# Performance work log

Measured on AMD Instinct MI355X. Metric: run time of the kernel, lower is better.

Reference implementation:

```python
import jax, jax.numpy as jnp
from jax import lax
import numpy as np

DN = ('NCHW', 'OIHW', 'NCHW')


def _conv(x, w, b, stride, pad):
    y = lax.conv_general_dilated(x, w, (stride, stride), [(pad, pad), (pad, pad)],
                                 dimension_numbers=DN)
    return y + b[None, :, None, None]


def _conv_t(x, w, b):
    # torch ConvTranspose2d(k=4, stride=2, padding=1) equivalent:
    # lhs_dilation=2, effective padding k-1-p = 2 on each side -> output 2H x 2W
    y = lax.conv_general_dilated(x, w, (1, 1), [(2, 2), (2, 2)],
                                 lhs_dilation=(2, 2), dimension_numbers=DN)
    return y + b[None, :, None, None]


def setup_inputs() -> dict:
    key = jax.random.key(0)
    ks = jax.random.split(key, 16)
    D, K = 8, 512  # latent_dim, codebook_size

    def w(k, shape, fan_in):
        return jax.random.normal(k, shape, jnp.float32) * (1.0 / np.sqrt(fan_in))

    inp = {
        'x': jax.random.uniform(ks[0], (32, 3, 256, 256), jnp.float32),
        # encoder
        'enc_w1': w(ks[1], (32, 3, 4, 4), 3 * 16), 'enc_b1': jnp.zeros((32,), jnp.float32),
        'enc_w2': w(ks[2], (64, 32, 4, 4), 32 * 16), 'enc_b2': jnp.zeros((64,), jnp.float32),
        'enc_w3': w(ks[3], (D, 64, 1, 1), 64), 'enc_b3': jnp.zeros((D,), jnp.float32),
        # codebook, uniform(-1/K, 1/K) as in torch init
        'codebook': jax.random.uniform(ks[4], (K, D), jnp.float32, -1.0 / K, 1.0 / K),
        # decoder
        'dec_w1': w(ks[5], (64, D, 3, 3), D * 9), 'dec_b1': jnp.zeros((64,), jnp.float32),
        'dect_w1': w(ks[6], (64, 64, 4, 4), 64 * 16), 'dect_b1': jnp.zeros((64,), jnp.float32),
        'dect_w2': w(ks[7], (32, 64, 4, 4), 64 * 16), 'dect_b2': jnp.zeros((32,), jnp.float32),
        'dec_w2': w(ks[8], (3, 32, 3, 3), 32 * 9), 'dec_b2': jnp.zeros((3,), jnp.float32),
    }
    return inp


def reference(x, enc_w1, enc_b1, enc_w2, enc_b2, enc_w3, enc_b3, codebook,
              dec_w1, dec_b1, dect_w1, dect_b1, dect_w2, dect_b2, dec_w2, dec_b2):
    commitment_cost = 0.25
    B = x.shape[0]
    D = codebook.shape[1]

    # encoder
    h = jax.nn.relu(_conv(x, enc_w1, enc_b1, 2, 1))
    h = jax.nn.relu(_conv(h, enc_w2, enc_b2, 2, 1))
    z = _conv(h, enc_w3, enc_b3, 1, 0)                      # [B, D, H/4, W/4]

    # VQ: pairwise squared distances, argmin, gather
    z_flat = z.transpose(0, 2, 3, 1).reshape(-1, D)          # [N, D] in NHWC order
    distances = (jnp.sum(z_flat ** 2, axis=1, keepdims=True)
                 + jnp.sum(codebook ** 2, axis=1)
                 - 2.0 * z_flat @ codebook.T)                 # [N, K]
    encoding_indices = jnp.argmin(distances, axis=1)          # [N]
    # NOTE: faithful to original bug - reshaped directly into NCHW without permute
    z_q = codebook[encoding_indices].reshape(z.shape)

    commitment_loss = jnp.mean((z - lax.stop_gradient(z_q)) ** 2)
    codebook_loss = jnp.mean((z_q - lax.stop_gradient(z)) ** 2)
    vq_loss = codebook_loss + commitment_cost * commitment_loss

    # straight-through estimator
    z_q = z + lax.stop_gradient(z_q - z)

    # decoder
    h = jax.nn.relu(_conv(z_q, dec_w1, dec_b1, 1, 1))
    h = jax.nn.relu(_conv_t(h, dect_w1, dect_b1))
    h = jax.nn.relu(_conv_t(h, dect_w2, dect_b2))
    x_recon = jax.nn.sigmoid(_conv(h, dec_w2, dec_b2, 1, 1))

    return x_recon, vq_loss, encoding_indices.reshape(B, -1)
```

## Files before the change

kernel.cpp:

```cpp
#include <hip/hip_runtime.h>
#include <hip/hip_bf16.h>
#include <math.h>


__device__ __forceinline__ int rfl(int v) { return __builtin_amdgcn_readfirstlane(v); }

typedef __attribute__((ext_vector_type(8))) short s8v;
typedef __attribute__((ext_vector_type(4))) float f4v;

__device__ __forceinline__ ushort f2bf(float f) {
    __hip_bfloat16 h = __float2bfloat16(f);
    return *(ushort*)&h;
}

__global__ __launch_bounds__(256) void k_conv1(const float* __restrict__ x, const float* __restrict__ w,
                                               const float* __restrict__ bias, float* __restrict__ out) {
    int t = blockIdx.x * 256 + threadIdx.x;
    int ow  = t & 127;
    int oh0 = ((t >> 7) & 31) * 4;
    int co0 = rfl((t >> 12) & 15);
    int b   = rfl(t >> 16);
    float acc[4][2] = {};
    for (int ci = 0; ci < 3; ci++) {
        const float* xp  = x + (b * 3 + ci) * 65536;
        const float* wpA = w + (co0 * 3 + ci) * 16;
        const float* wpB = w + ((co0 + 16) * 3 + ci) * 16;
        #pragma unroll
        for (int r = 0; r < 10; r++) {
            int ih = oh0 * 2 - 1 + r;
            bool rok = (ih >= 0) && (ih < 256);
            int ihc = rok ? ih : 0;
            float v[4];
            #pragma unroll
            for (int c = 0; c < 4; c++) {
                int iw = ow * 2 - 1 + c;
                bool ok = rok && (iw >= 0) && (iw < 256);
                int iwc = iw < 0 ? 0 : (iw > 255 ? 255 : iw);
                float vv = xp[ihc * 256 + iwc];
                v[c] = ok ? vv : 0.f;
            }
            #pragma unroll
            for (int o = 0; o < 4; o++) {
                int kh = r - 2 * o;
                if (kh >= 0 && kh < 4) {
                    #pragma unroll
                    for (int kw = 0; kw < 4; kw++) {
                        acc[o][0] = __builtin_fmaf(v[kw], wpA[kh * 4 + kw], acc[o][0]);
                        acc[o][1] = __builtin_fmaf(v[kw], wpB[kh * 4 + kw], acc[o][1]);
                    }
                }
            }
        }
    }
    float bA = bias[co0], bB = bias[co0 + 16];
    #pragma unroll
    for (int o = 0; o < 4; o++) {
        float vA = acc[o][0] + bA, vB = acc[o][1] + bB;
        out[((b * 32 + co0) * 128 + oh0 + o) * 128 + ow]      = vA > 0.f ? vA : 0.f;
        out[((b * 32 + co0 + 16) * 128 + oh0 + o) * 128 + ow] = vB > 0.f ? vB : 0.f;
    }
}

__global__ __launch_bounds__(256) void k_conv2t(const float* __restrict__ h1, const float* __restrict__ w,
                                                const float* __restrict__ bias, float* __restrict__ out) {
    __shared__ float P[32][18][2][10];
    int bx = blockIdx.x;
    int b  = bx >> 6;
    int ty = (bx >> 3) & 7, tx = bx & 7;
    int oh0 = ty * 8, ow0 = tx * 8;
    int tid = threadIdx.x;
    for (int i = tid; i < 10368; i += 256) {
        int ci = i / 324, rem = i - ci * 324;
        int r = rem / 18, c = rem - r * 18;
        int ih = oh0 * 2 - 1 + r, iw = ow0 * 2 - 1 + c;
        float v = 0.f;
        if (ih >= 0 && ih < 128 && iw >= 0 && iw < 128)
            v = h1[(b * 32 + ci) * 16384 + ih * 128 + iw];
        P[ci][r][c & 1][c >> 1] = v;
    }
    __syncthreads();
    int lane = tid & 63;
    int dy = lane >> 3, dx = lane & 7;
    int co_base = rfl((tid >> 6) * 16);
    int oh = oh0 + dy, ow = ow0 + dx;
    for (int cc = 0; cc < 4; cc++) {
        int co0 = co_base + cc * 4;
        float a0 = 0.f, a1 = 0.f, a2 = 0.f, a3 = 0.f;
        for (int ci = 0; ci < 32; ci++) {
            const float* wp0 = w + ((co0 + 0) * 32 + ci) * 16;
            const float* wp1 = w + ((co0 + 1) * 32 + ci) * 16;
            const float* wp2 = w + ((co0 + 2) * 32 + ci) * 16;
            const float* wp3 = w + ((co0 + 3) * 32 + ci) * 16;
            #pragma unroll
            for (int kh = 0; kh < 4; kh++) {
                int r = 2 * dy + kh;
                float v0 = P[ci][r][0][dx];
                float v1 = P[ci][r][1][dx];
                float v2 = P[ci][r][0][dx + 1];
                float v3 = P[ci][r][1][dx + 1];
                a0 = __builtin_fmaf(v0, wp0[kh*4+0], a0); a0 = __builtin_fmaf(v1, wp0[kh*4+1], a0);
                a0 = __builtin_fmaf(v2, wp0[kh*4+2], a0); a0 = __builtin_fmaf(v3, wp0[kh*4+3], a0);
                a1 = __builtin_fmaf(v0, wp1[kh*4+0], a1); a1 = __builtin_fmaf(v1, wp1[kh*4+1], a1);
                a1 = __builtin_fmaf(v2, wp1[kh*4+2], a1); a1 = __builtin_fmaf(v3, wp1[kh*4+3], a1);
                a2 = __builtin_fmaf(v0, wp2[kh*4+0], a2); a2 = __builtin_fmaf(v1, wp2[kh*4+1], a2);
                a2 = __builtin_fmaf(v2, wp2[kh*4+2], a2); a2 = __builtin_fmaf(v3, wp2[kh*4+3], a2);
                a3 = __builtin_fmaf(v0, wp3[kh*4+0], a3); a3 = __builtin_fmaf(v1, wp3[kh*4+1], a3);
                a3 = __builtin_fmaf(v2, wp3[kh*4+2], a3); a3 = __builtin_fmaf(v3, wp3[kh*4+3], a3);
            }
        }
        float r0 = a0 + bias[co0 + 0], r1 = a1 + bias[co0 + 1];
        float r2 = a2 + bias[co0 + 2], r3 = a3 + bias[co0 + 3];
        out[((b * 64 + co0 + 0) * 64 + oh) * 64 + ow] = r0 > 0.f ? r0 : 0.f;
        out[((b * 64 + co0 + 1) * 64 + oh) * 64 + ow] = r1 > 0.f ? r1 : 0.f;
        out[((b * 64 + co0 + 2) * 64 + oh) * 64 + ow] = r2 > 0.f ? r2 : 0.f;
        out[((b * 64 + co0 + 3) * 64 + oh) * 64 + ow] = r3 > 0.f ? r3 : 0.f;
    }
}

__global__ __launch_bounds__(256) void k_conv3(const float* __restrict__ h2, const float* __restrict__ w,
                                               const float* __restrict__ bias, float* __restrict__ zf) {
    __shared__ float wl[8][64];
    __shared__ float bl[8];
    int tid = threadIdx.x;
    for (int i = tid; i < 512; i += 256) wl[i >> 6][i & 63] = w[i];
    if (tid < 8) bl[tid] = bias[tid];
    __syncthreads();
    int t = blockIdx.x * 256 + tid;
    int b = t >> 12, hw = t & 4095;
    float acc[8];
    for (int d = 0; d < 8; d++) acc[d] = 0.f;
    for (int ci = 0; ci < 64; ci++) {
        float v = h2[(b * 64 + ci) * 4096 + hw];
        for (int d = 0; d < 8; d++) acc[d] = __builtin_fmaf(v, wl[d][ci], acc[d]);
    }
    for (int d = 0; d < 8; d++)
        zf[(b * 8 + d) * 4096 + hw] = acc[d] + bl[d];
}

__global__ __launch_bounds__(256) void k_vq(const float* __restrict__ zf, const float* __restrict__ cb,
                                            int* __restrict__ idx, float* __restrict__ out_idx) {
    __shared__ float cbs[512][8];
    __shared__ float c2s[512];
    int tid = threadIdx.x;
    for (int i = tid; i < 4096; i += 256) cbs[i >> 3][i & 7] = cb[i];
    __syncthreads();
    for (int k = tid; k < 512; k += 256) {
        float s = 0.f;
        for (int d = 0; d < 8; d++) {
            float c = cbs[k][d];
            s = s + __fmul_rn(c, c);
        }
        c2s[k] = s;
    }
    __syncthreads();
    int n = blockIdx.x * 256 + tid;
    int b = n >> 12, hw = n & 4095;
    float zv[8], s1 = 0.f;
    for (int d = 0; d < 8; d++) {
        float z = zf[(b * 8 + d) * 4096 + hw];
        zv[d] = z;
        s1 = s1 + __fmul_rn(z, z);
    }
    float best = 3.4e38f; int bi = 0;
    for (int k = 0; k < 512; k++) {
        float dot = 0.f;
        for (int d = 0; d < 8; d++) dot = __builtin_fmaf(zv[d], cbs[k][d], dot);
        float a = s1 + c2s[k];
        float dist = a - __fmul_rn(2.0f, dot);
        if (dist < best) { best = dist; bi = k; }
    }
    idx[n] = bi;
    out_idx[n] = (float)bi;
}

__global__ __launch_bounds__(256) void k_zq(const int* __restrict__ idx, const float* __restrict__ cb,
                                            const float* __restrict__ zf, float* __restrict__ zq,
                                            double* __restrict__ partial) {
    __shared__ double red[256];
    int t = blockIdx.x * 256 + threadIdx.x;
    float q = cb[idx[t >> 3] * 8 + (t & 7)];
    zq[t] = q;
    double d = (double)zf[t] - (double)q;
    red[threadIdx.x] = d * d;
    __syncthreads();
    for (int s = 128; s > 0; s >>= 1) {
        if (threadIdx.x < s) red[threadIdx.x] += red[threadIdx.x + s];
        __syncthreads();
    }
    if (threadIdx.x == 0) partial[blockIdx.x] = red[0];
}

__global__ __launch_bounds__(256) void k_loss_fin(const double* __restrict__ partial, float* __restrict__ out_loss) {
    __shared__ double red[256];
    double s = 0.0;
    for (int i = threadIdx.x; i < 4096; i += 256) s += partial[i];
    red[threadIdx.x] = s;
    __syncthreads();
    for (int st = 128; st > 0; st >>= 1) {
        if (threadIdx.x < st) red[threadIdx.x] += red[threadIdx.x + st];
        __syncthreads();
    }
    if (threadIdx.x == 0)
        out_loss[0] = (float)(1.25 * red[0] / 1048576.0);
}

__global__ __launch_bounds__(256) void k_dec1(const float* __restrict__ zq, const float* __restrict__ w,
                                              const float* __restrict__ bias, float* __restrict__ out) {
    int t = blockIdx.x * 256 + threadIdx.x;
    int ow  = t & 63;
    int oh0 = ((t >> 6) & 15) * 4;
    int co0 = rfl((t >> 10) & 31);
    int b   = rfl(t >> 15);
    float acc[4][2] = {};
    for (int ci = 0; ci < 8; ci++) {
        const float* ip  = zq + (b * 8 + ci) * 4096;
        const float* wpA = w + (co0 * 8 + ci) * 9;
        const float* wpB = w + ((co0 + 32) * 8 + ci) * 9;
        #pragma unroll
        for (int r = 0; r < 6; r++) {
            int ih = oh0 - 1 + r;
            bool rok = (ih >= 0) && (ih < 64);
            int ihc = rok ? ih : 0;
            float v[3];
            #pragma unroll
            for (int c = 0; c < 3; c++) {
                int iw = ow - 1 + c;
                bool ok = rok && (iw >= 0) && (iw < 64);
                int iwc = iw < 0 ? 0 : (iw > 63 ? 63 : iw);
                float vv = ip[ihc * 64 + iwc];
                v[c] = ok ? vv : 0.f;
            }
            #pragma unroll
            for (int o = 0; o < 4; o++) {
                int kh = r - o;
                if (kh >= 0 && kh < 3) {
                    #pragma unroll
                    for (int kw = 0; kw < 3; kw++) {
                        acc[o][0] = __builtin_fmaf(v[kw], wpA[kh * 3 + kw], acc[o][0]);
                        acc[o][1] = __builtin_fmaf(v[kw], wpB[kh * 3 + kw], acc[o][1]);
                    }
                }
            }
        }
    }
    float bA = bias[co0], bB = bias[co0 + 32];
    #pragma unroll
    for (int o = 0; o < 4; o++) {
        float vA = acc[o][0] + bA, vB = acc[o][1] + bB;
        out[((b * 64 + co0) * 64 + oh0 + o) * 64 + ow]      = vA > 0.f ? vA : 0.f;
        out[((b * 64 + co0 + 32) * 64 + oh0 + o) * 64 + ow] = vB > 0.f ? vB : 0.f;
    }
}

template <int CI, int CO>
__global__ __launch_bounds__(256) void k_wprep(const float* __restrict__ w, ushort* __restrict__ Wf) {
    constexpr int NT = CO / 16;
    int t = blockIdx.x * 256 + threadIdx.x;
    if (t >= 4 * NT * 8 * 64) return;
    int lane = t & 63;
    int kt = (t >> 6) & 7;
    int nt = (t >> 9) % NT;
    int q  = t / (512 * NT);
    int py = q >> 1, px = q & 1;
    int n = nt * 16 + (lane & 15);
    int cb = (kt & 1) * 32 + (lane >> 4) * 8;
    int tap = kt >> 1, dy = tap >> 1, dx = tap & 1;
    #pragma unroll
    for (int jj = 0; jj < 8; jj++) {
        int ci = cb + jj;
        float v = w[((n * CI + ci) * 4 + (py + 2 * dy)) * 4 + (px + 2 * dx)];
        Wf[(((q * NT + nt) * 8 + kt) * 64 + lane) * 8 + jj] = f2bf(v);
    }
}

template <int CI, int CO, int HIN>
__global__ __launch_bounds__(256) void k_dect_mfma(const float* __restrict__ in, const ushort* __restrict__ Wf,
                                                   const float* __restrict__ bias, float* __restrict__ out) {
    constexpr int NT = CO / 16;
    constexpr int TILES = HIN / 16;
    constexpr int HOUT = 2 * HIN;
    __shared__ alignas(16) ushort L[18 * 18 * 72];
    int blk = blockIdx.x;
    int b = blk / (TILES * TILES);
    int tile = blk - b * (TILES * TILES);
    int i0 = (tile / TILES) * 16, j0 = (tile % TILES) * 16;
    const float* ip = in + (size_t)b * CI * HIN * HIN;
    for (int e = threadIdx.x; e < 18 * 18 * CI; e += 256) {
        int ci = e / 324; int rem = e - ci * 324;
        int row = rem / 18; int col = rem - row * 18;
        int ih = i0 - 1 + row, iw = j0 - 1 + col;
        float v = 0.f;
        if (ih >= 0 && ih < HIN && iw >= 0 && iw < HIN)
            v = ip[(size_t)ci * (HIN * HIN) + ih * HIN + iw];
        L[(row * 18 + col) * 72 + ci] = f2bf(v);
    }
    __syncthreads();
    int wv = threadIdx.x >> 6;
    int lane = threadIdx.x & 63;
    int py = wv >> 1, px = wv & 1;
    int m = lane & 15, quad = lane >> 4;
    const ushort* wq = Wf + (size_t)wv * NT * 8 * 64 * 8;
    for (int il = 0; il < 16; il++) {
        s8v a[8];
        #pragma unroll
        for (int kt = 0; kt < 8; kt++) {
            int tap = kt >> 1, dy = tap >> 1, dx = tap & 1;
            int r = il + py + dy, cl = m + px + dx;
            a[kt] = *(s8v*)&L[(r * 18 + cl) * 72 + (kt & 1) * 32 + quad * 8];
        }
        #pragma unroll
        for (int nt = 0; nt < NT; nt++) {
            f4v acc = {0.f, 0.f, 0.f, 0.f};
            #pragma unroll
            for (int kt = 0; kt < 8; kt++) {
                s8v bf = *(const s8v*)&wq[((nt * 8 + kt) * 64 + lane) * 8];
                acc = __builtin_amdgcn_mfma_f32_16x16x32_bf16(a[kt], bf, acc, 0, 0, 0);
            }
            int co = nt * 16 + m;
            float bv = bias[co];
            int y = 2 * (i0 + il) + py;
            #pragma unroll
            for (int reg = 0; reg < 4; reg++) {
                int jD = j0 + quad * 4 + reg;
                int xx = 2 * jD + px;
                float v = acc[reg] + bv;
                out[((size_t)(b * CO + co) * HOUT + y) * HOUT + xx] = v > 0.f ? v : 0.f;
            }
        }
    }
}

__global__ __launch_bounds__(256) void k_dec2(const float* __restrict__ in, const float* __restrict__ w,
                                              const float* __restrict__ bias, float* __restrict__ out) {
    int t = blockIdx.x * 256 + threadIdx.x;
    int x  = t & 255;
    int y0 = ((t >> 8) & 63) * 4;
    int r  = rfl(t >> 14);
    int co = r % 3, b = r / 3;
    float acc[4] = {};
    for (int ci = 0; ci < 32; ci++) {
        const float* ip = in + (size_t)(b * 32 + ci) * 65536;
        const float* wp = w + (co * 32 + ci) * 9;
        #pragma unroll
        for (int rr = 0; rr < 6; rr++) {
            int ih = y0 - 1 + rr;
            bool rok = (ih >= 0) && (ih < 256);
            int ihc = rok ? ih : 0;
            float v[3];
            #pragma unroll
            for (int c = 0; c < 3; c++) {
                int iw = x - 1 + c;
                bool ok = rok && (iw >= 0) && (iw < 256);
                int iwc = iw < 0 ? 0 : (iw > 255 ? 255 : iw);
                float vv = ip[ihc * 256 + iwc];
                v[c] = ok ? vv : 0.f;
            }
            #pragma unroll
            for (int o = 0; o < 4; o++) {
                int kh = rr - o;
                if (kh >= 0 && kh < 3) {
                    #pragma unroll
                    for (int kw = 0; kw < 3; kw++)
                        acc[o] = __builtin_fmaf(v[kw], wp[kh * 3 + kw], acc[o]);
                }
            }
        }
    }
    float bv = bias[co];
    #pragma unroll
    for (int o = 0; o < 4; o++) {
        float v = acc[o] + bv;
        out[((size_t)(b * 3 + co) * 256 + y0 + o) * 256 + x] = 1.0f / (1.0f + expf(-v));
    }
}

extern "C" void kernel_launch(void* const* d_in, const int* in_sizes, int n_in,
                              void* d_out, int out_size, void* d_ws, size_t ws_size,
                              hipStream_t stream) {
    const float* x    = (const float*)d_in[0];
    const float* ew1  = (const float*)d_in[1];
    const float* eb1  = (const float*)d_in[2];
    const float* ew2  = (const float*)d_in[3];
    const float* eb2  = (const float*)d_in[4];
    const float* ew3  = (const float*)d_in[5];
    const float* eb3  = (const float*)d_in[6];
    const float* cb   = (const float*)d_in[7];
    const float* dw1  = (const float*)d_in[8];
    const float* db1  = (const float*)d_in[9];
    const float* dtw1 = (const float*)d_in[10];
    const float* dtb1 = (const float*)d_in[11];
    const float* dtw2 = (const float*)d_in[12];
    const float* dtb2 = (const float*)d_in[13];
    const float* dw2  = (const float*)d_in[14];
    const float* db2  = (const float*)d_in[15];

    char* ws = (char*)d_ws;
    float*  z32  = (float*) (ws);
    float*  zq   = (float*) (ws + 4194304);
    int*    idx  = (int*)   (ws + 8388608);
    double* part = (double*)(ws + 8912896);
    ushort* Wf1  = (ushort*)(ws + 8945664);
    ushort* Wf2  = (ushort*)(ws + 9076736);
    char* region = ws + 9142272;

    size_t fixed = 9142272;
    size_t avail = (ws_size > fixed) ? ws_size - fixed : 0;
    int ce = 32, cd = 32;
    while (ce > 1 && (size_t)ce * 3145728ull > avail) ce >>= 1;
    while (cd > 1 && (size_t)cd * 13631488ull > avail) cd >>= 1;

    float* h1c = (float*)region;
    float* h2c = (float*)(region + (size_t)ce * 2097152ull);
    float* d3c = (float*) region;
    float* d4c = (float*) (region + (size_t)cd * 1048576ull);
    float* d5c = (float*) (region + (size_t)cd * 5242880ull);

    float* out      = (float*)d_out;
    float* out_loss = out + 6291456;
    float* out_idx  = out + 6291457;

    for (int c = 0; c < 32 / ce; c++) {
        const float* xc = x + (size_t)c * ce * 196608ull;
        k_conv1<<<ce * 256, 256, 0, stream>>>(xc, ew1, eb1, h1c);
        k_conv2t<<<ce * 64, 256, 0, stream>>>(h1c, ew2, eb2, h2c);
        k_conv3<<<ce * 16,  256, 0, stream>>>(h2c, ew3, eb3, z32 + (size_t)c * ce * 32768ull);
    }

    k_vq<<<512, 256, 0, stream>>>(z32, cb, idx, out_idx);
    k_zq<<<4096, 256, 0, stream>>>(idx, cb, z32, zq, part);
    k_loss_fin<<<1, 256, 0, stream>>>(part, out_loss);

    k_wprep<64, 64><<<32, 256, 0, stream>>>(dtw1, Wf1);
    k_wprep<64, 32><<<16, 256, 0, stream>>>(dtw2, Wf2);

    for (int c = 0; c < 32 / cd; c++) {
        const float* zqc = zq + (size_t)c * cd * 32768ull;
        float* outc = out + (size_t)c * cd * 196608ull;
        k_dec1<<<cd * 128, 256, 0, stream>>>(zqc, dw1, db1, d3c);
        k_dect_mfma<64, 64, 64 ><<<cd * 16, 256, 0, stream>>>(d3c, Wf1, dtb1, d4c);
        k_dect_mfma<64, 32, 128><<<cd * 64, 256, 0, stream>>>(d4c, Wf2, dtb2, d5c);
        k_dec2<<<cd * 192, 256, 0, stream>>>(d5c, dw2, db2, outc);
    }
}
```

Baseline: 1.079 ms.

## Compute more output channels per thread in direct conv kernels

Four direct convolution kernels (conv1, conv2t, dec1, dec2) now accumulate more output channels per thread (8, 16, 8 and 3 respectively), so each loaded input value is reused across more channels and the input is re-read fewer times. conv2t now stages input channels into shared memory in two halves of 16, which halves the LDS footprint. Grid sizes shrink to match. This cuts redundant global and LDS input loads, but it raises register pressure and reduces the number of blocks, which could lower occupancy.

```diff
diff --git a/kernel.cpp b/kernel.cpp
--- a/kernel.cpp
+++ b/kernel.cpp
@@ -18,13 +18,12 @@
     int t = blockIdx.x * 256 + threadIdx.x;
     int ow  = t & 127;
     int oh0 = ((t >> 7) & 31) * 4;
-    int co0 = rfl((t >> 12) & 15);
-    int b   = rfl(t >> 16);
-    float acc[4][2] = {};
+    int co0 = rfl((t >> 12) & 3) * 8;
+    int b   = rfl(t >> 14);
+    float acc[4][8] = {};
     for (int ci = 0; ci < 3; ci++) {
-        const float* xp  = x + (b * 3 + ci) * 65536;
-        const float* wpA = w + (co0 * 3 + ci) * 16;
-        const float* wpB = w + ((co0 + 16) * 3 + ci) * 16;
+        const float* xp = x + (b * 3 + ci) * 65536;
+        const float* wp = w + (co0 * 3 + ci) * 16;
         #pragma unroll
         for (int r = 0; r < 10; r++) {
             int ih = oh0 * 2 - 1 + r;
@@ -44,76 +43,78 @@
                 int kh = r - 2 * o;
                 if (kh >= 0 && kh < 4) {
                     #pragma unroll
-                    for (int kw = 0; kw < 4; kw++) {
-                        acc[o][0] = __builtin_fmaf(v[kw], wpA[kh * 4 + kw], acc[o][0]);
-                        acc[o][1] = __builtin_fmaf(v[kw], wpB[kh * 4 + kw], acc[o][1]);
+                    for (int cc = 0; cc < 8; cc++) {
+                        const float* wc = wp + cc * 48 + kh * 4;
+                        acc[o][cc] = __builtin_fmaf(v[0], wc[0], acc[o][cc]);
+                        acc[o][cc] = __builtin_fmaf(v[1], wc[1], acc[o][cc]);
+                        acc[o][cc] = __builtin_fmaf(v[2], wc[2], acc[o][cc]);
+                        acc[o][cc] = __builtin_fmaf(v[3], wc[3], acc[o][cc]);
                     }
                 }
             }
         }
     }
-    float bA = bias[co0], bB = bias[co0 + 16];
     #pragma unroll
-    for (int o = 0; o < 4; o++) {
-        float vA = acc[o][0] + bA, vB = acc[o][1] + bB;
-        out[((b * 32 + co0) * 128 + oh0 + o) * 128 + ow]      = vA > 0.f ? vA : 0.f;
-        out[((b * 32 + co0 + 16) * 128 + oh0 + o) * 128 + ow] = vB > 0.f ? vB : 0.f;
+    for (int cc = 0; cc < 8; cc++) {
+        float bv = bias[co0 + cc];
+        #pragma unroll
+        for (int o = 0; o < 4; o++) {
+            float v = acc[o][cc] + bv;
+            out[((b * 32 + co0 + cc) * 128 + oh0 + o) * 128 + ow] = v > 0.f ? v : 0.f;
+        }
     }
 }
 
 __global__ __launch_bounds__(256) void k_conv2t(const float* __restrict__ h1, const float* __restrict__ w,
                                                 const float* __restrict__ bias, float* __restrict__ out) {
-    __shared__ float P[32][18][2][10];
+    __shared__ float P[16][18][2][10];
     int bx = blockIdx.x;
     int b  = bx >> 6;
     int ty = (bx >> 3) & 7, tx = bx & 7;
     int oh0 = ty * 8, ow0 = tx * 8;
     int tid = threadIdx.x;
-    for (int i = tid; i < 10368; i += 256) {
-        int ci = i / 324, rem = i - ci * 324;
-        int r = rem / 18, c = rem - r * 18;
-        int ih = oh0 * 2 - 1 + r, iw = ow0 * 2 - 1 + c;
-        float v = 0.f;
-        if (ih >= 0 && ih < 128 && iw >= 0 && iw < 128)
-            v = h1[(b * 32 + ci) * 16384 + ih * 128 + iw];
-        P[ci][r][c & 1][c >> 1] = v;
-    }
-    __syncthreads();
     int lane = tid & 63;
     int dy = lane >> 3, dx = lane & 7;
-    int co_base = rfl((tid >> 6) * 16);
+    int co0 = rfl(tid >> 6) * 16;
     int oh = oh0 + dy, ow = ow0 + dx;
-    for (int cc = 0; cc < 4; cc++) {
-        int co0 = co_base + cc * 4;
-        float a0 = 0.f, a1 = 0.f, a2 = 0.f, a3 = 0.f;
-        for (int ci = 0; ci < 32; ci++) {
-            const float* wp0 = w + ((co0 + 0) * 32 + ci) * 16;
-            const float* wp1 = w + ((co0 + 1) * 32 + ci) * 16;
-            const float* wp2 = w + ((co0 + 2) * 32 + ci) * 16;
-            const float* wp3 = w + ((co0 + 3) * 32 + ci) * 16;
+    float acc[16] = {};
+    for (int pass = 0; pass < 2; pass++) {
+        int cib = pass * 16;
+        __syncthreads();
+        for (int i = tid; i < 16 * 18 * 18; i += 256) {
+            int cl = i / 324, rem = i - cl * 324;
+            int r = rem / 18, c = rem - r * 18;
+            int ih = oh0 * 2 - 1 + r, iw = ow0 * 2 - 1 + c;
+            float v = 0.f;
+            if (ih >= 0 && ih < 128 && iw >= 0 && iw < 128)
+                v = h1[(b * 32 + cib + cl) * 16384 + ih * 128 + iw];
+            P[cl][r][c & 1][c >> 1] = v;
+        }
+        __syncthreads();
+        for (int cl = 0; cl < 16; cl++) {
+            const float* wp = w + (co0 * 32 + cib + cl) * 16;
             #pragma unroll
             for (int kh = 0; kh < 4; kh++) {
                 int r = 2 * dy + kh;
-                float v0 = P[ci][r][0][dx];
-                float v1 = P[ci][r][1][dx];
-                float v2 = P[ci][r][0][dx + 1];
-                float v3 = P[ci][r][1][dx + 1];
-                a0 = __builtin_fmaf(v0, wp0[kh*4+0], a0); a0 = __builtin_fmaf(v1, wp0[kh*4+1], a0);
-                a0 = __builtin_fmaf(v2, wp0[kh*4+2], a0); a0 = __builtin_fmaf(v3, wp0[kh*4+3], a0);
-                a1 = __builtin_fmaf(v0, wp1[kh*4+0], a1); a1 = __builtin_fmaf(v1, wp1[kh*4+1], a1);
-                a1 = __builtin_fmaf(v2, wp1[kh*4+2], a1); a1 = __builtin_fmaf(v3, wp1[kh*4+3], a1);
-                a2 = __builtin_fmaf(v0, wp2[kh*4+0], a2); a2 = __builtin_fmaf(v1, wp2[kh*4+1], a2);
-                a2 = __builtin_fmaf(v2, wp2[kh*4+2], a2); a2 = __builtin_fmaf(v3, wp2[kh*4+3], a2);
-                a3 = __builtin_fmaf(v0, wp3[kh*4+0], a3); a3 = __builtin_fmaf(v1, wp3[kh*4+1], a3);
-                a3 = __builtin_fmaf(v2, wp3[kh*4+2], a3); a3 = __builtin_fmaf(v3, wp3[kh*4+3], a3);
-            }
-        }
-        float r0 = a0 + bias[co0 + 0], r1 = a1 + bias[co0 + 1];
-        float r2 = a2 + bias[co0 + 2], r3 = a3 + bias[co0 + 3];
-        out[((b * 64 + co0 + 0) * 64 + oh) * 64 + ow] = r0 > 0.f ? r0 : 0.f;
-        out[((b * 64 + co0 + 1) * 64 + oh) * 64 + ow] = r1 > 0.f ? r1 : 0.f;
-        out[((b * 64 + co0 + 2) * 64 + oh) * 64 + ow] = r2 > 0.f ? r2 : 0.f;
-        out[((b * 64 + co0 + 3) * 64 + oh) * 64 + ow] = r3 > 0.f ? r3 : 0.f;
+                float v0 = P[cl][r][0][dx];
+                float v1 = P[cl][r][1][dx];
+                float v2 = P[cl][r][0][dx + 1];
+                float v3 = P[cl][r][1][dx + 1];
+                #pragma unroll
+                for (int c = 0; c < 16; c++) {
+                    const float* wc = wp + c * 512 + kh * 4;
+                    acc[c] = __builtin_fmaf(v0, wc[0], acc[c]);
+                    acc[c] = __builtin_fmaf(v1, wc[1], acc[c]);
+                    acc[c] = __builtin_fmaf(v2, wc[2], acc[c]);
+                    acc[c] = __builtin_fmaf(v3, wc[3], acc[c]);
+                }
+            }
+        }
+    }
+    #pragma unroll
+    for (int c = 0; c < 16; c++) {
+        float v = acc[c] + bias[co0 + c];
+        out[((b * 64 + co0 + c) * 64 + oh) * 64 + ow] = v > 0.f ? v : 0.f;
     }
 }
 
@@ -209,13 +210,12 @@
     int t = blockIdx.x * 256 + threadIdx.x;
     int ow  = t & 63;
     int oh0 = ((t >> 6) & 15) * 4;
-    int co0 = rfl((t >> 10) & 31);
-    int b   = rfl(t >> 15);
-    float acc[4][2] = {};
+    int co0 = rfl((t >> 10) & 7) * 8;
+    int b   = rfl(t >> 13);
+    float acc[4][8] = {};
     for (int ci = 0; ci < 8; ci++) {
-        const float* ip  = zq + (b * 8 + ci) * 4096;
-        const float* wpA = w + (co0 * 8 + ci) * 9;
-        const float* wpB = w + ((co0 + 32) * 8 + ci) * 9;
+        const float* ip = zq + (b * 8 + ci) * 4096;
+        const float* wp = w + (co0 * 8 + ci) * 9;
         #pragma unroll
         for (int r = 0; r < 6; r++) {
             int ih = oh0 - 1 + r;
@@ -235,20 +235,24 @@
                 int kh = r - o;
                 if (kh >= 0 && kh < 3) {
                     #pragma unroll
-                    for (int kw = 0; kw < 3; kw++) {
-                        acc[o][0] = __builtin_fmaf(v[kw], wpA[kh * 3 + kw], acc[o][0]);
-                        acc[o][1] = __builtin_fmaf(v[kw], wpB[kh * 3 + kw], acc[o][1]);
+                    for (int cc = 0; cc < 8; cc++) {
+                        const float* wc = wp + cc * 72 + kh * 3;
+                        acc[o][cc] = __builtin_fmaf(v[0], wc[0], acc[o][cc]);
+                        acc[o][cc] = __builtin_fmaf(v[1], wc[1], acc[o][cc]);
+                        acc[o][cc] = __builtin_fmaf(v[2], wc[2], acc[o][cc]);
                     }
                 }
             }
         }
     }
-    float bA = bias[co0], bB = bias[co0 + 32];
     #pragma unroll
-    for (int o = 0; o < 4; o++) {
-        float vA = acc[o][0] + bA, vB = acc[o][1] + bB;
-        out[((b * 64 + co0) * 64 + oh0 + o) * 64 + ow]      = vA > 0.f ? vA : 0.f;
-        out[((b * 64 + co0 + 32) * 64 + oh0 + o) * 64 + ow] = vB > 0.f ? vB : 0.f;
+    for (int cc = 0; cc < 8; cc++) {
+        float bv = bias[co0 + cc];
+        #pragma unroll
+        for (int o = 0; o < 4; o++) {
+            float v = acc[o][cc] + bv;
+            out[((b * 64 + co0 + cc) * 64 + oh0 + o) * 64 + ow] = v > 0.f ? v : 0.f;
+        }
     }
 }
 
@@ -335,12 +339,11 @@
     int t = blockIdx.x * 256 + threadIdx.x;
     int x  = t & 255;
     int y0 = ((t >> 8) & 63) * 4;
-    int r  = rfl(t >> 14);
-    int co = r % 3, b = r / 3;
-    float acc[4] = {};
+    int b  = rfl(t >> 14);
+    float acc[4][3] = {};
     for (int ci = 0; ci < 32; ci++) {
         const float* ip = in + (size_t)(b * 32 + ci) * 65536;
-        const float* wp = w + (co * 32 + ci) * 9;
+        const float* wp = w + ci * 9;
         #pragma unroll
         for (int rr = 0; rr < 6; rr++) {
             int ih = y0 - 1 + rr;
@@ -360,17 +363,24 @@
                 int kh = rr - o;
                 if (kh >= 0 && kh < 3) {
                     #pragma unroll
-                    for (int kw = 0; kw < 3; kw++)
-                        acc[o] = __builtin_fmaf(v[kw], wp[kh * 3 + kw], acc[o]);
+                    for (int co = 0; co < 3; co++) {
+                        const float* wc = wp + co * 288 + kh * 3;
+                        acc[o][co] = __builtin_fmaf(v[0], wc[0], acc[o][co]);
+                        acc[o][co] = __builtin_fmaf(v[1], wc[1], acc[o][co]);
+                        acc[o][co] = __builtin_fmaf(v[2], wc[2], acc[o][co]);
+                    }
                 }
             }
         }
     }
-    float bv = bias[co];
     #pragma unroll
-    for (int o = 0; o < 4; o++) {
-        float v = acc[o] + bv;
-        out[((size_t)(b * 3 + co) * 256 + y0 + o) * 256 + x] = 1.0f / (1.0f + expf(-v));
+    for (int co = 0; co < 3; co++) {
+        float bv = bias[co];
+        #pragma unroll
+        for (int o = 0; o < 4; o++) {
+            float v = acc[o][co] + bv;
+            out[((size_t)(b * 3 + co) * 256 + y0 + o) * 256 + x] = 1.0f / (1.0f + expf(-v));
+        }
     }
 }
 
@@ -421,7 +431,7 @@
 
     for (int c = 0; c < 32 / ce; c++) {
         const float* xc = x + (size_t)c * ce * 196608ull;
-        k_conv1<<<ce * 256, 256, 0, stream>>>(xc, ew1, eb1, h1c);
+        k_conv1<<<ce * 64, 256, 0, stream>>>(xc, ew1, eb1, h1c);
         k_conv2t<<<ce * 64, 256, 0, stream>>>(h1c, ew2, eb2, h2c);
         k_conv3<<<ce * 16,  256, 0, stream>>>(h2c, ew3, eb3, z32 + (size_t)c * ce * 32768ull);
     }
@@ -436,9 +446,9 @@
     for (int c = 0; c < 32 / cd; c++) {
         const float* zqc = zq + (size_t)c * cd * 32768ull;
         float* outc = out + (size_t)c * cd * 196608ull;
-        k_dec1<<<cd * 128, 256, 0, stream>>>(zqc, dw1, db1, d3c);
+        k_dec1<<<cd * 32, 256, 0, stream>>>(zqc, dw1, db1, d3c);
         k_dect_mfma<64, 64, 64 ><<<cd * 16, 256, 0, stream>>>(d3c, Wf1, dtb1, d4c);
         k_dect_mfma<64, 32, 128><<<cd * 64, 256, 0, stream>>>(d4c, Wf2, dtb2, d5c);
-        k_dec2<<<cd * 192, 256, 0, stream>>>(d5c, dw2, db2, outc);
-    }
-}
+        k_dec2<<<cd * 64, 256, 0, stream>>>(d5c, dw2, db2, outc);
+    }
+}
```

After: 1.055 ms. 2.2% less time.
